# Kernel optimization log

Measured on AMD Instinct MI355X. Metric: run time of the kernel, lower is better.

Reference implementation:

```python
import jax, jax.numpy as jnp
import numpy as np

N, E, D, H = 20000, 160000, 64, 4  # nodes, edges, hidden_dim, heads
C = D  # per-head out channels (concat=False -> mean over heads)
NEG_SLOPE = 0.2


def _mlp2(x, w1, b1, w2, b2):
    return jax.nn.relu(x @ w1 + b1) @ w2 + b2


def _gatv2(h, e_full, src, dst, wl, bl, wr, br, we, att, bias):
    # GATv2Conv (PyG semantics, share_weights=False, concat=False)
    xl = (h @ wl + bl).reshape(N, H, C)          # lin_l (source / message features)
    xr = (h @ wr + br).reshape(N, H, C)          # lin_r (target features)
    ee = (e_full @ we).reshape(-1, H, C)         # lin_edge (no bias)
    m = jax.nn.leaky_relu(xl[src] + xr[dst] + ee, NEG_SLOPE)  # [E',H,C]
    logits = jnp.einsum('ehc,hc->eh', m, att)    # [E',H]
    # segment softmax over destination node neighborhoods
    mx = jax.ops.segment_max(logits, dst, num_segments=N)
    ex = jnp.exp(logits - mx[dst])
    s = jax.ops.segment_sum(ex, dst, num_segments=N)
    alpha = ex / s[dst]                          # [E',H]
    out = jax.ops.segment_sum(xl[src] * alpha[..., None], dst, num_segments=N)
    return out.mean(axis=1) + bias               # [N,D]


def setup_inputs() -> dict:
    key = jax.random.key(0)
    ks = iter(jax.random.split(key, 40))
    nrm = lambda shape, s=0.05: jax.random.normal(next(ks), shape, jnp.float32) * s
    inp = {
        'x': jax.random.normal(next(ks), (N, 2), jnp.float32),
        'edge_index': jax.random.randint(next(ks), (2, E), 0, N, dtype=jnp.int32),
        'edge_attr': jax.random.normal(next(ks), (E, 3), jnp.float32),
        # node encoder
        'ne_w1': nrm((2, D)), 'ne_b1': jnp.zeros((D,), jnp.float32),
        'ne_w2': nrm((D, D)), 'ne_b2': jnp.zeros((D,), jnp.float32),
        # edge encoder
        'ee_w1': nrm((3, D)), 'ee_b1': jnp.zeros((D,), jnp.float32),
        'ee_w2': nrm((D, D)), 'ee_b2': jnp.zeros((D,), jnp.float32),
        # 3 GATv2Conv layers, params stacked along leading layer dim
        'cv_wl': nrm((3, D, H * C)), 'cv_bl': jnp.zeros((3, H * C), jnp.float32),
        'cv_wr': nrm((3, D, H * C)), 'cv_br': jnp.zeros((3, H * C), jnp.float32),
        'cv_we': nrm((3, D, H * C)),
        'cv_att': nrm((3, H, C)),
        'cv_bias': jnp.zeros((3, D), jnp.float32),
        # edge classifier (3D -> D -> 1)
        'ec_w1': nrm((3 * D, D)), 'ec_b1': jnp.zeros((D,), jnp.float32),
        'ec_w2': nrm((D, 1)), 'ec_b2': jnp.zeros((1,), jnp.float32),
        'or_w1': nrm((D, D)), 'or_b1': jnp.zeros((D,), jnp.float32),
        'or_w2': nrm((D, 2)), 'or_b2': jnp.zeros((2,), jnp.float32),
    }
    return inp


def reference(x, edge_index, edge_attr,
              ne_w1, ne_b1, ne_w2, ne_b2,
              ee_w1, ee_b1, ee_w2, ee_b2,
              cv_wl, cv_bl, cv_wr, cv_br, cv_we, cv_att, cv_bias,
              ec_w1, ec_b1, ec_w2, ec_b2,
              or_w1, or_b1, or_w2, or_b2):
    src, dst = edge_index[0], edge_index[1]
    h = _mlp2(x, ne_w1, ne_b1, ne_w2, ne_b2)          # [N,D]
    e = _mlp2(edge_attr, ee_w1, ee_b1, ee_w2, ee_b2)  # [E,D]
    # PyG add_self_loops with fill_value='mean': loop attr = mean of incoming edge attrs
    cnt = jax.ops.segment_sum(jnp.ones((E,), e.dtype), dst, num_segments=N)
    e_loop = jax.ops.segment_sum(e, dst, num_segments=N) / jnp.clip(cnt, 1.0)[:, None]
    loop = jnp.arange(N, dtype=src.dtype)
    src_f = jnp.concatenate([src, loop])
    dst_f = jnp.concatenate([dst, loop])
    e_f = jnp.concatenate([e, e_loop], axis=0)        # [E+N,D]
    for l in range(3):
        h = h + jax.nn.relu(_gatv2(h, e_f, src_f, dst_f,
                                   cv_wl[l], cv_bl[l], cv_wr[l], cv_br[l],
                                   cv_we[l], cv_att[l], cv_bias[l]))
    edge_feat = jnp.concatenate([h[src], h[dst], e], axis=1)  # [E,3D]
    edge_scores = jax.nn.sigmoid(_mlp2(edge_feat, ec_w1, ec_b1, ec_w2, ec_b2)).squeeze(-1)
    pred_offsets = _mlp2(h, or_w1, or_b1, or_w2, or_b2)       # [N,2]
    return (edge_scores, pred_offsets)
```

## Files before the change

### kernel.cpp

```cpp
#include <hip/hip_runtime.h>

#define N_NODES 20000
#define N_EDGES 160000
#define EP (N_EDGES + N_NODES)
#define NBLK ((N_NODES + 255) / 256)
#define PREP_SEG 16384
#define EENC_BLK (N_EDGES / 64)
#define ECLS_BLK (N_EDGES / 64)

typedef __attribute__((ext_vector_type(8))) short bf16x8;
typedef __attribute__((ext_vector_type(4))) float f32x4;

__device__ __forceinline__ short f2bf(float f) {
  unsigned u = __float_as_uint(f);
  unsigned r = (u + 0x7FFFu + ((u >> 16) & 1u)) >> 16;
  return (short)r;
}
__device__ __forceinline__ float b2f(short s) {
  return __uint_as_float(((unsigned)(unsigned short)s) << 16);
}

__device__ __forceinline__ f32x4 mfma16(bf16x8 a, bf16x8 b, f32x4 c) {
  return __builtin_amdgcn_mfma_f32_16x16x32_bf16(a, b, c, 0, 0, 0);
}

__device__ __forceinline__ float bcast(float v, int k) {
  return __uint_as_float(__builtin_amdgcn_readlane(__float_as_uint(v), k));
}

__device__ __forceinline__ float wred_sum(float v) {
#pragma unroll
  for (int o = 32; o > 0; o >>= 1) v += __shfl_xor(v, o, 64);
  return v;
}

__device__ __forceinline__ void gl16(const short* g, short* l) {
  __builtin_amdgcn_global_load_lds(
      (const __attribute__((address_space(1))) void*)g,
      (__attribute__((address_space(3))) void*)l, 16, 0, 0);
}

__global__ void k_prep_all(const float* __restrict__ cv_wl, const float* __restrict__ cv_wr,
                           const float* __restrict__ cv_we, const float* __restrict__ ec_w1,
                           const float* __restrict__ ee_w2,
                           short* __restrict__ wlf, short* __restrict__ wrf,
                           short* __restrict__ wef, short* __restrict__ updf,
                           short* __restrict__ eclsf, short* __restrict__ encf,
                           int* __restrict__ cnt, int* __restrict__ fill) {
  int i = blockIdx.x * 256 + threadIdx.x;
  if (i < 12 * PREP_SEG) {
    int grp = i / PREP_SEG;
    int r = i % PREP_SEG;
    int kind = grp / 3, l = grp % 3;
    int j = r & 7, lane = (r >> 3) & 63;
    int q = lane & 15, g = lane >> 4;
    if (kind < 3) {
      int kh = (r >> 9) & 1, t = (r >> 10) & 3, w = r >> 12;
      int k = kh * 32 + g * 8 + j, c = w * 64 + t * 16 + q;
      const float* W = (kind == 0 ? cv_wl : kind == 1 ? cv_wr : cv_we) + (size_t)l * 64 * 256;
      short* out = (kind == 0 ? wlf : kind == 1 ? wrf : wef) + (size_t)l * PREP_SEG;
      out[r] = f2bf(W[k * 256 + c]);
    } else {
      int kh = (r >> 9) & 7, w = r >> 12;
      int k = kh * 32 + g * 8 + j, c = w * 16 + q;
      const float* W = cv_wl + (size_t)l * 64 * 256;
      updf[(size_t)l * PREP_SEG + r] = f2bf(0.25f * W[(k & 63) * 256 + (k >> 6) * 64 + c]);
    }
  } else if (i < 12 * PREP_SEG + 12288) {
    int r = i - 12 * PREP_SEG;
    int j = r & 7, lane = (r >> 3) & 63, f = r >> 9;
    int w = f / 6, kh = f % 6;
    int q = lane & 15, g = lane >> 4;
    int k = kh * 32 + g * 8 + j, c = w * 16 + q;
    eclsf[r] = f2bf(ec_w1[(size_t)k * 64 + c]);
  } else if (i < 12 * PREP_SEG + 12288 + 4096) {
    int r = i - 12 * PREP_SEG - 12288;
    int j = r & 7, lane = (r >> 3) & 63, f = r >> 9;
    int w = f >> 1, kh = f & 1;
    int q = lane & 15, g = lane >> 4;
    int k = kh * 32 + g * 8 + j, c = w * 16 + q;
    encf[r] = f2bf(ee_w2[(size_t)k * 64 + c]);
  } else {
    int r = i - (12 * PREP_SEG + 12288 + 4096);
    if (r < N_NODES) cnt[r] = 0;
    else if (r < 2 * N_NODES) fill[r - N_NODES] = 0;
  }
}


__global__ void k_count(const int* __restrict__ dst, int* __restrict__ cnt) {
  int i = blockIdx.x * blockDim.x + threadIdx.x;
  if (i < N_EDGES) atomicAdd(&cnt[dst[i]], 1);
}

__global__ void k_scan1(const int* __restrict__ cnt, int* __restrict__ row_ptr,
                        int* __restrict__ bsum) {
  __shared__ int sh[256];
  int t = threadIdx.x, b = blockIdx.x, i = b * 256 + t;
  int v = (i < N_NODES) ? cnt[i] + 1 : 0;
  sh[t] = v;
  __syncthreads();
#pragma unroll
  for (int off = 1; off < 256; off <<= 1) {
    int x = (t >= off) ? sh[t - off] : 0;
    __syncthreads();
    sh[t] += x;
    __syncthreads();
  }
  if (i < N_NODES) row_ptr[i + 1] = sh[t];
  if (t == 255) bsum[b] = sh[255];
}

__global__ void k_scan2(const int* __restrict__ bsum, int* __restrict__ boff) {
  __shared__ int sh[256];
  int t = threadIdx.x;
  int v = (t < NBLK) ? bsum[t] : 0;
  sh[t] = v;
  __syncthreads();
#pragma unroll
  for (int off = 1; off < 256; off <<= 1) {
    int x = (t >= off) ? sh[t - off] : 0;
    __syncthreads();
    sh[t] += x;
    __syncthreads();
  }
  if (t < NBLK) boff[t] = sh[t] - v;
}

__global__ void k_scan3(const int* __restrict__ boff, int* __restrict__ row_ptr) {
  int t = threadIdx.x, b = blockIdx.x, i = b * 256 + t;
  if (i < N_NODES) row_ptr[i + 1] += boff[b];
  if (i == 0) row_ptr[0] = 0;
}

__global__ void k_scatter(const int* __restrict__ dst, const int* __restrict__ row_ptr,
                          int* __restrict__ fill, int* __restrict__ col_idx,
                          int* __restrict__ pdst) {
  int i = blockIdx.x * blockDim.x + threadIdx.x;
  if (i >= EP) return;
  int d = (i < N_EDGES) ? dst[i] : (i - N_EDGES);
  int p = row_ptr[d] + atomicAdd(&fill[d], 1);
  col_idx[p] = i;
  pdst[p] = d;
}

__global__ void k_sortp(const int* __restrict__ row_ptr, int* __restrict__ col_idx,
                        const int* __restrict__ src, int* __restrict__ psrc,
                        int* __restrict__ pos) {
  int n = blockIdx.x * blockDim.x + threadIdx.x;
  if (n >= N_NODES) return;
  int s = row_ptr[n], e = row_ptr[n + 1];
  for (int i = s + 1; i < e; ++i) {
    int v = col_idx[i];
    int j = i - 1;
    while (j >= s && col_idx[j] > v) { col_idx[j + 1] = col_idx[j]; --j; }
    col_idx[j + 1] = v;
  }
  for (int i = s; i < e; ++i) {
    int eid = col_idx[i];
    pos[eid] = i;
    psrc[i] = (eid < N_EDGES) ? src[eid] : (eid - N_EDGES);
  }
}


__global__ __launch_bounds__(256) void k_enc(
    const float* __restrict__ x,
    const float* __restrict__ nw1, const float* __restrict__ nb1,
    const float* __restrict__ nw2, const float* __restrict__ nb2,
    const float* __restrict__ ea,
    const float* __restrict__ ew1, const float* __restrict__ eb1,
    const short* __restrict__ encf, const float* __restrict__ eb2,
    const int* __restrict__ pos, short* __restrict__ efc,
    float* __restrict__ h, short* __restrict__ hb) {
  __shared__ __align__(16) char smraw[17920];
  int tid = threadIdx.x;
  int lane = tid & 63, w = tid >> 6, q = lane & 15, g = lane >> 4;
  if (blockIdx.x < EENC_BLK) {
    short* hs = (short*)smraw;
    short* ot = (short*)(smraw + 9216);
    int* ps = (int*)(smraw + 9216 + 8192);
    int e0 = blockIdx.x * 64;
    if (tid < 64) ps[tid] = pos[e0 + tid];
    float w1a = ew1[lane], w1b = ew1[64 + lane], w1c = ew1[128 + lane], b1v = eb1[lane];
#pragma unroll
    for (int t = 0; t < 16; ++t) {
      int e = w * 16 + t;
      float a0 = ea[(size_t)(e0 + e) * 3];
      float a1 = ea[(size_t)(e0 + e) * 3 + 1];
      float a2 = ea[(size_t)(e0 + e) * 3 + 2];
      float hid = fmaxf(a0 * w1a + a1 * w1b + a2 * w1c + b1v, 0.f);
      hs[e * 72 + lane] = f2bf(hid);
    }
    bf16x8 A0 = *(const bf16x8*)&hs[(w * 16 + q) * 72 + g * 8];
    bf16x8 A1 = *(const bf16x8*)&hs[(w * 16 + q) * 72 + 32 + g * 8];
#pragma unroll
    for (int cc = 0; cc < 4; ++cc) {
      bf16x8 B0 = *(const bf16x8*)(encf + ((size_t)(cc * 2 + 0) * 64 + lane) * 8);
      bf16x8 B1 = *(const bf16x8*)(encf + ((size_t)(cc * 2 + 1) * 64 + lane) * 8);
      f32x4 z = {0.f, 0.f, 0.f, 0.f};
      z = mfma16(A0, B0, z);
      z = mfma16(A1, B1, z);
      float bv = eb2[cc * 16 + q];
#pragma unroll
      for (int r = 0; r < 4; ++r)
        ot[(w * 16 + g * 4 + r) * 64 + cc * 16 + q] = f2bf(z[r] + bv);
    }
    __syncthreads();
    int row = tid >> 2, part = tid & 3;
    short* d = efc + (size_t)ps[row] * 64 + part * 16;
    const short* s = ot + row * 64 + part * 16;
    *(bf16x8*)d = *(const bf16x8*)s;
    *(bf16x8*)(d + 8) = *(const bf16x8*)(s + 8);
  } else {
    float* w2l = (float*)smraw;
#pragma unroll
    for (int qq = 0; qq < 16; ++qq) w2l[qq * 256 + tid] = nw2[qq * 256 + tid];
    __syncthreads();
    int n = (blockIdx.x - EENC_BLK) * 4 + w;
    float x0 = x[n * 2], x1 = x[n * 2 + 1];
    float hid = fmaxf(x0 * nw1[lane] + x1 * nw1[64 + lane] + nb1[lane], 0.f);
    float out = nb2[lane];
#pragma unroll
    for (int k = 0; k < 64; ++k) out += bcast(hid, k) * w2l[k * 64 + lane];
    h[n * 64 + lane] = out;
    hb[n * 64 + lane] = f2bf(out);
  }
}

__global__ __launch_bounds__(256) void k_loop_feat(
    const int* __restrict__ row_ptr, short* __restrict__ efc) {
  int tid = threadIdx.x, lane = tid & 63, w = tid >> 6;
  int n = blockIdx.x * 4 + w;
  int s = row_ptr[n], e1 = row_ptr[n + 1];
  int r8 = lane >> 3, oct = lane & 7;
  float acc[8];
#pragma unroll
  for (int j = 0; j < 8; ++j) acc[j] = 0.f;
  for (int p0 = s; p0 < e1 - 1; p0 += 8) {
    int p = p0 + r8;
    if (p < e1 - 1) {
      bf16x8 A = *(const bf16x8*)(efc + (size_t)p * 64 + oct * 8);
#pragma unroll
      for (int j = 0; j < 8; ++j) acc[j] += b2f(A[j]);
    }
  }
#pragma unroll
  for (int j = 0; j < 8; ++j) {
    acc[j] += __shfl_xor(acc[j], 8, 64);
    acc[j] += __shfl_xor(acc[j], 16, 64);
    acc[j] += __shfl_xor(acc[j], 32, 64);
  }
  int c = e1 - 1 - s;
  float invc = 1.f / (float)(c > 0 ? c : 1);
  if (lane < 8) {
    bf16x8 o8;
#pragma unroll
    for (int j = 0; j < 8; ++j) o8[j] = f2bf(acc[j] * invc);
    *(bf16x8*)(efc + (size_t)(e1 - 1) * 64 + lane * 8) = o8;
  }
}


__global__ __launch_bounds__(256) void k_elog(
    const short* __restrict__ hb, const short* __restrict__ efc,
    const int* __restrict__ psrc, const int* __restrict__ pdst,
    const short* __restrict__ wlf, const short* __restrict__ wrf,
    const short* __restrict__ wef, const float* __restrict__ bl,
    const float* __restrict__ br, const float* __restrict__ att, float* __restrict__ lg) {
  __shared__ __align__(16) short smA[96 * 2 * 64];
  int tid = threadIdx.x;
  int w = tid >> 6, lane = tid & 63, q = lane & 15, g = lane >> 4;
  int cbase = w * 64;
  int pb = blockIdx.x * 96;

  int id6[6];
#pragma unroll
  for (int j = 0; j < 6; ++j) {
    int s = (w * 6 + j) * 64 + lane;
    int t = s >> 8, s2 = s & 255;
    int r = s2 >> 7, e = (s2 >> 3) & 15;
    int pe = pb + t * 16 + e;
    id6[j] = (r == 0) ? psrc[pe] : pe;
  }
#pragma unroll
  for (int j = 0; j < 6; ++j) {
    int s = (w * 6 + j) * 64 + lane;
    int s2 = s & 255;
    int r = s2 >> 7, e = (s2 >> 3) & 15, c16 = s & 7;
    int cs = (c16 ^ (e & 7)) * 8;
    const short* gp = ((r == 1) ? efc : hb) + (size_t)id6[j] * 64 + cs;
    gl16(gp, &smA[(size_t)s * 8]);
  }

  int nd[6];
#pragma unroll
  for (int t = 0; t < 6; ++t) nd[t] = pdst[pb + t * 16 + q];

  bf16x8 Bl[4][2], Br[4][2], Be[4][2];
  float av[4], bv[4];
#pragma unroll
  for (int t = 0; t < 4; ++t) {
    int c = cbase + t * 16 + q;
    av[t] = att[c];
    bv[t] = bl[c] + br[c];
#pragma unroll
    for (int kh = 0; kh < 2; ++kh) {
      size_t fo = ((size_t)((w * 4 + t) * 2 + kh) * 64 + lane) * 8;
      Bl[t][kh] = *(const bf16x8*)(wlf + fo);
      Br[t][kh] = *(const bf16x8*)(wrf + fo);
      Be[t][kh] = *(const bf16x8*)(wef + fo);
    }
  }
  __syncthreads();

  int xa = (g ^ (q & 7)) * 8;
  int xb = ((4 + g) ^ (q & 7)) * 8;
  int rowoff = q * 64;
#pragma unroll
  for (int t = 0; t < 6; ++t) {
    const short* base = smA + t * 2048;
    const short* ar = hb + (size_t)nd[t] * 64;
    bf16x8 As0 = *(const bf16x8*)(base + rowoff + xa);
    bf16x8 As1 = *(const bf16x8*)(base + rowoff + xb);
    bf16x8 Ar0 = *(const bf16x8*)(ar + g * 8);
    bf16x8 Ar1 = *(const bf16x8*)(ar + 32 + g * 8);
    bf16x8 Ae0 = *(const bf16x8*)(base + 1024 + rowoff + xa);
    bf16x8 Ae1 = *(const bf16x8*)(base + 1024 + rowoff + xb);
    f32x4 acc[4];
#pragma unroll
    for (int tt = 0; tt < 4; ++tt) {
      f32x4 z = {0.f, 0.f, 0.f, 0.f};
      z = mfma16(As0, Bl[tt][0], z);
      z = mfma16(As1, Bl[tt][1], z);
      z = mfma16(Ar0, Br[tt][0], z);
      z = mfma16(Ar1, Br[tt][1], z);
      z = mfma16(Ae0, Be[tt][0], z);
      acc[tt] = mfma16(Ae1, Be[tt][1], z);
    }
#pragma unroll
    for (int r = 0; r < 4; ++r) {
      float pd = 0.f;
#pragma unroll
      for (int tt = 0; tt < 4; ++tt) {
        float m = acc[tt][r] + bv[tt];
        m = m > 0.f ? m : 0.2f * m;
        pd += m * av[tt];
      }
      pd += __shfl_xor(pd, 1, 64);
      pd += __shfl_xor(pd, 2, 64);
      pd += __shfl_xor(pd, 4, 64);
      pd += __shfl_xor(pd, 8, 64);
      if (q == 0) lg[(size_t)(pb + t * 16 + g * 4 + r) * 4 + w] = pd;
    }
  }
}

__global__ __launch_bounds__(256) void k_aggupd(
    const short* __restrict__ hbin, const float* __restrict__ lg,
    const int* __restrict__ row_ptr, const int* __restrict__ psrc,
    const short* __restrict__ updf, const float* __restrict__ bl,
    const float* __restrict__ bias, float* __restrict__ h, short* __restrict__ hbout) {
  __shared__ short agls[16 * 264];
  __shared__ float albuf[4][260];
  int tid = threadIdx.x, lane = tid & 63, w = tid >> 6;
  int q = lane & 15, g = lane >> 4;
  int n0 = blockIdx.x * 16;
  int i16 = lane & 15, h4 = lane >> 4;
  float* alw = albuf[w];
#pragma unroll 1
  for (int i = 0; i < 4; ++i) {
    int n = n0 + w * 4 + i;
    int s0 = row_ptr[n], s1 = row_ptr[n + 1];
    float m = -3.4e38f;
    for (int p = s0 + i16; p < s1; p += 16) m = fmaxf(m, lg[(size_t)p * 4 + h4]);
#pragma unroll
    for (int o = 1; o < 16; o <<= 1) m = fmaxf(m, __shfl_xor(m, o, 64));
    float sum = 0.f;
    for (int p = s0 + i16; p < s1; p += 16) sum += __expf(lg[(size_t)p * 4 + h4] - m);
#pragma unroll
    for (int o = 1; o < 16; o <<= 1) sum += __shfl_xor(sum, o, 64);
    float inv = 1.f / sum;
    float ih4[4];
#pragma unroll
    for (int hh = 0; hh < 4; ++hh) ih4[hh] = __shfl(inv, hh * 16, 64);
    float acc[4][4];
#pragma unroll
    for (int hh = 0; hh < 4; ++hh)
#pragma unroll
      for (int j = 0; j < 4; ++j) acc[hh][j] = 0.f;
    for (int wst = s0; wst < s1; wst += 64) {
      int wend = wst + 64 < s1 ? wst + 64 : s1;
#pragma unroll
      for (int k = 0; k < 4; ++k) {
        int p = wst + k * 16 + i16;
        float e = (p < s1) ? __expf(lg[(size_t)p * 4 + h4] - m) : 0.f;
        alw[(k * 16 + i16) * 4 + h4] = e;
      }
      asm volatile("s_waitcnt lgkmcnt(0)" ::: "memory");
      for (int p0 = wst; p0 < wend; p0 += 4) {
        int p = p0 + h4;
        bool v = p < wend;
        int pc = v ? p : wend - 1;
        int sp = psrc[pc];
        float4 al = *(const float4*)&alw[(pc - wst) * 4];
        short4 hv = *(const short4*)(hbin + (size_t)sp * 64 + i16 * 4);
        if (!v) { al.x = 0.f; al.y = 0.f; al.z = 0.f; al.w = 0.f; }
        float hf0 = b2f(hv.x), hf1 = b2f(hv.y), hf2 = b2f(hv.z), hf3 = b2f(hv.w);
        acc[0][0] += al.x * hf0; acc[0][1] += al.x * hf1;
        acc[0][2] += al.x * hf2; acc[0][3] += al.x * hf3;
        acc[1][0] += al.y * hf0; acc[1][1] += al.y * hf1;
        acc[1][2] += al.y * hf2; acc[1][3] += al.y * hf3;
        acc[2][0] += al.z * hf0; acc[2][1] += al.z * hf1;
        acc[2][2] += al.z * hf2; acc[2][3] += al.z * hf3;
        acc[3][0] += al.w * hf0; acc[3][1] += al.w * hf1;
        acc[3][2] += al.w * hf2; acc[3][3] += al.w * hf3;
      }
    }
#pragma unroll
    for (int hh = 0; hh < 4; ++hh)
#pragma unroll
      for (int j = 0; j < 4; ++j) {
        acc[hh][j] += __shfl_xor(acc[hh][j], 16, 64);
        acc[hh][j] += __shfl_xor(acc[hh][j], 32, 64);
      }
    if (lane < 16) {
#pragma unroll
      for (int hh = 0; hh < 4; ++hh) {
        short4 o4;
        o4.x = f2bf(acc[hh][0] * ih4[hh]);
        o4.y = f2bf(acc[hh][1] * ih4[hh]);
        o4.z = f2bf(acc[hh][2] * ih4[hh]);
        o4.w = f2bf(acc[hh][3] * ih4[hh]);
        *(short4*)(agls + (w * 4 + i) * 264 + hh * 64 + i16 * 4) = o4;
      }
    }
  }
  __syncthreads();
  const short* arow = agls + q * 264;
  f32x4 z = {0.f, 0.f, 0.f, 0.f};
#pragma unroll
  for (int kh = 0; kh < 8; ++kh) {
    bf16x8 A = *(const bf16x8*)(arow + kh * 32 + g * 8);
    bf16x8 B = *(const bf16x8*)(updf + ((size_t)(w * 8 + kh) * 64 + lane) * 8);
    z = mfma16(A, B, z);
  }
  int c = w * 16 + q;
  float bf = 0.25f * (bl[c] + bl[64 + c] + bl[128 + c] + bl[192 + c]) + bias[c];
#pragma unroll
  for (int r = 0; r < 4; ++r) {
    int n = n0 + g * 4 + r;
    float nh = h[(size_t)n * 64 + c] + fmaxf(z[r] + bf, 0.f);
    h[(size_t)n * 64 + c] = nh;
    hbout[(size_t)n * 64 + c] = f2bf(nh);
  }
}

__global__ __launch_bounds__(256) void k_heads(
    const short* __restrict__ hb, const short* __restrict__ efc,
    const int* __restrict__ src, const int* __restrict__ dst,
    const int* __restrict__ pos, const short* __restrict__ eclsf,
    const float* __restrict__ b1, const float* __restrict__ w2,
    const float* __restrict__ b2,
    const float* __restrict__ h, const float* __restrict__ ow1,
    const float* __restrict__ ob1, const float* __restrict__ ow2,
    const float* __restrict__ ob2, float* __restrict__ out) {
  __shared__ __align__(16) char smraw[25600];
  int tid = threadIdx.x;
  int w = tid >> 6, lane = tid & 63, q = lane & 15, g = lane >> 4;
  if (blockIdx.x < ECLS_BLK) {
    short* smA = (short*)smraw;
    float* sm = (float*)(smraw + 24576);
    int e0b = blockIdx.x * 64;
    int id6[6];
#pragma unroll
    for (int j = 0; j < 6; ++j) {
      int s = (w * 6 + j) * 64 + lane;
      int r = s >> 9, e = (s >> 3) & 63;
      int eg = e0b + e;
      id6[j] = (r == 0) ? src[eg] : (r == 1) ? dst[eg] : pos[eg];
    }
#pragma unroll
    for (int j = 0; j < 6; ++j) {
      int s = (w * 6 + j) * 64 + lane;
      int r = s >> 9, e = (s >> 3) & 63, c16 = s & 7;
      int cs = (c16 ^ (e & 7)) * 8;
      const short* gp = ((r == 2) ? efc : hb) + (size_t)id6[j] * 64 + cs;
      gl16(gp, &smA[(size_t)s * 8]);
    }
    int c = w * 16 + q;
    bf16x8 Bf[6];
#pragma unroll
    for (int kh = 0; kh < 6; ++kh)
      Bf[kh] = *(const bf16x8*)(eclsf + ((size_t)(w * 6 + kh) * 64 + lane) * 8);
    float b1v = b1[c], w2v = w2[c], b2v = b2[0];
    __syncthreads();
    int xa = (g ^ (q & 7)) * 8;
    int xb = ((4 + g) ^ (q & 7)) * 8;
#pragma unroll
    for (int tile = 0; tile < 4; ++tile) {
      const short* rp = smA + (tile * 16 + q) * 64;
      f32x4 acc = {0.f, 0.f, 0.f, 0.f};
      acc = mfma16(*(const bf16x8*)(rp + xa), Bf[0], acc);
      acc = mfma16(*(const bf16x8*)(rp + xb), Bf[1], acc);
      acc = mfma16(*(const bf16x8*)(rp + 4096 + xa), Bf[2], acc);
      acc = mfma16(*(const bf16x8*)(rp + 4096 + xb), Bf[3], acc);
      acc = mfma16(*(const bf16x8*)(rp + 8192 + xa), Bf[4], acc);
      acc = mfma16(*(const bf16x8*)(rp + 8192 + xb), Bf[5], acc);
#pragma unroll
      for (int r = 0; r < 4; ++r) {
        float hv = fmaxf(acc[r] + b1v, 0.f) * w2v;
        hv += __shfl_xor(hv, 1, 64);
        hv += __shfl_xor(hv, 2, 64);
        hv += __shfl_xor(hv, 4, 64);
        hv += __shfl_xor(hv, 8, 64);
        if (q == 0) sm[tile * 64 + w * 16 + g * 4 + r] = hv;
      }
    }
    __syncthreads();
    if (tid < 64) {
      int tile = tid >> 4, e = tid & 15;
      float t = sm[tile * 64 + e] + sm[tile * 64 + 16 + e] +
                sm[tile * 64 + 32 + e] + sm[tile * 64 + 48 + e] + b2v;
      out[e0b + tile * 16 + e] = 1.f / (1.f + __expf(-t));
    }
  } else {
    float* w1l = (float*)smraw;
#pragma unroll
    for (int qq = 0; qq < 16; ++qq) w1l[qq * 256 + tid] = ow1[qq * 256 + tid];
    __syncthreads();
    int n = (blockIdx.x - ECLS_BLK) * 4 + w;
    float hr = h[n * 64 + lane];
    float hid = ob1[lane];
#pragma unroll
    for (int k = 0; k < 64; ++k) hid += bcast(hr, k) * w1l[k * 64 + lane];
    hid = fmaxf(hid, 0.f);
    float p0 = wred_sum(hid * ow2[lane * 2]);
    float p1 = wred_sum(hid * ow2[lane * 2 + 1]);
    if (lane == 0) {
      out[N_EDGES + n * 2] = p0 + ob2[0];
      out[N_EDGES + n * 2 + 1] = p1 + ob2[1];
    }
  }
}


extern "C" void kernel_launch(void* const* d_in, const int* in_sizes, int n_in,
                              void* d_out, int out_size, void* d_ws, size_t ws_size,
                              hipStream_t stream) {
  const float* x     = (const float*)d_in[0];
  const int*   eidx  = (const int*)d_in[1];
  const float* eattr = (const float*)d_in[2];
  const float* ne_w1 = (const float*)d_in[3];
  const float* ne_b1 = (const float*)d_in[4];
  const float* ne_w2 = (const float*)d_in[5];
  const float* ne_b2 = (const float*)d_in[6];
  const float* ee_w1 = (const float*)d_in[7];
  const float* ee_b1 = (const float*)d_in[8];
  const float* ee_w2 = (const float*)d_in[9];
  const float* ee_b2 = (const float*)d_in[10];
  const float* cv_wl = (const float*)d_in[11];
  const float* cv_bl = (const float*)d_in[12];
  const float* cv_wr = (const float*)d_in[13];
  const float* cv_br = (const float*)d_in[14];
  const float* cv_we = (const float*)d_in[15];
  const float* cv_att = (const float*)d_in[16];
  const float* cv_bias = (const float*)d_in[17];
  const float* ec_w1 = (const float*)d_in[18];
  const float* ec_b1 = (const float*)d_in[19];
  const float* ec_w2 = (const float*)d_in[20];
  const float* ec_b2 = (const float*)d_in[21];
  const float* or_w1 = (const float*)d_in[22];
  const float* or_b1 = (const float*)d_in[23];
  const float* or_w2 = (const float*)d_in[24];
  const float* or_b2 = (const float*)d_in[25];

  const int* src = eidx;
  const int* dst = eidx + N_EDGES;

  float* fws = (float*)d_ws;
  size_t o = 0;
  float* h  = fws + o; o += (size_t)N_NODES * 64;
  float* lg = fws + o; o += (size_t)EP * 4;
  short* sws = (short*)(fws + o);
  size_t so = 0;
  short* hb0  = sws + so; so += (size_t)N_NODES * 64;
  short* hb1  = sws + so; so += (size_t)N_NODES * 64;
  short* efc  = sws + so; so += (size_t)EP * 64;
  short* wlf  = sws + so; so += 3 * PREP_SEG;
  short* wrf  = sws + so; so += 3 * PREP_SEG;
  short* wef  = sws + so; so += 3 * PREP_SEG;
  short* updf = sws + so; so += 3 * PREP_SEG;
  short* eclsf = sws + so; so += 12288;
  short* encf  = sws + so; so += 4096;
  int* iws = (int*)(sws + so + (so & 1));
  int* row_ptr = iws;
  int* col_idx = iws + (N_NODES + 64);
  int* pdst = col_idx + EP;
  int* psrc = pdst + EP;
  int* pos  = psrc + EP;
  int* cnt  = pos + EP;
  int* fill = cnt + N_NODES;
  int* bsum = fill + N_NODES;
  int* boff = bsum + 128;

  float* out = (float*)d_out;

  k_prep_all<<<(12 * PREP_SEG + 12288 + 4096 + 2 * N_NODES + 255) / 256, 256, 0, stream>>>(
      cv_wl, cv_wr, cv_we, ec_w1, ee_w2, wlf, wrf, wef, updf, eclsf, encf, cnt, fill);

  k_count<<<(N_EDGES + 255) / 256, 256, 0, stream>>>(dst, cnt);
  k_scan1<<<NBLK, 256, 0, stream>>>(cnt, row_ptr, bsum);
  k_scan2<<<1, 256, 0, stream>>>(bsum, boff);
  k_scan3<<<NBLK, 256, 0, stream>>>(boff, row_ptr);
  k_scatter<<<(EP + 255) / 256, 256, 0, stream>>>(dst, row_ptr, fill, col_idx, pdst);
  k_sortp<<<(N_NODES + 255) / 256, 256, 0, stream>>>(row_ptr, col_idx, src, psrc, pos);

  k_enc<<<EENC_BLK + N_NODES / 4, 256, 0, stream>>>(
      x, ne_w1, ne_b1, ne_w2, ne_b2, eattr, ee_w1, ee_b1, encf, ee_b2, pos, efc, h, hb0);
  k_loop_feat<<<N_NODES / 4, 256, 0, stream>>>(row_ptr, efc);

  short* hcur = hb0;
  short* hnxt = hb1;
  for (int l = 0; l < 3; ++l) {
    const float* bl = cv_bl + (size_t)l * 256;
    const float* br = cv_br + (size_t)l * 256;
    const float* at = cv_att + (size_t)l * 256;
    const float* bi = cv_bias + (size_t)l * 64;
    k_elog<<<EP / 96, 256, 0, stream>>>(hcur, efc, psrc, pdst,
                                        wlf + (size_t)l * PREP_SEG,
                                        wrf + (size_t)l * PREP_SEG,
                                        wef + (size_t)l * PREP_SEG, bl, br, at, lg);
    k_aggupd<<<N_NODES / 16, 256, 0, stream>>>(hcur, lg, row_ptr, psrc,
                                               updf + (size_t)l * PREP_SEG, bl, bi, h, hnxt);
    short* tmp = hcur; hcur = hnxt; hnxt = tmp;
  }

  k_heads<<<ECLS_BLK + N_NODES / 4, 256, 0, stream>>>(
      hcur, efc, src, dst, pos, eclsf, ec_b1, ec_w2, ec_b2,
      h, or_w1, or_b1, or_w2, or_b2, out);
}
```

Baseline: 283.9 us.

## Fuse scan kernels, stage edge attrs in LDS, fold softmax sum into aggregation

Merges the second and third prefix-scan kernels into one single-block kernel that applies block offsets to row_ptr, removing one launch. The edge encoder loads edge attributes cooperatively into shared memory instead of doing strided per-thread global loads. The aggregation kernel computes the softmax denominator during the weighted-sum pass rather than in a separate pass over the logits. Leaky ReLU becomes fmaxf. The single-block offset pass runs serially over 20000 entries on one CU, which may cost more than the launch it removes.

New measurement: 283.8 us, median of 2. Within noise of the previous version (-0.0%).

```diff
diff --git a/kernel.cpp b/kernel.cpp
--- a/kernel.cpp
+++ b/kernel.cpp
@@ -111,8 +111,9 @@
   if (t == 255) bsum[b] = sh[255];
 }
 
-__global__ void k_scan2(const int* __restrict__ bsum, int* __restrict__ boff) {
+__global__ void k_scan23(const int* __restrict__ bsum, int* __restrict__ row_ptr) {
   __shared__ int sh[256];
+  __shared__ int boffs[128];
   int t = threadIdx.x;
   int v = (t < NBLK) ? bsum[t] : 0;
   sh[t] = v;
@@ -124,13 +125,10 @@
     sh[t] += x;
     __syncthreads();
   }
-  if (t < NBLK) boff[t] = sh[t] - v;
-}
-
-__global__ void k_scan3(const int* __restrict__ boff, int* __restrict__ row_ptr) {
-  int t = threadIdx.x, b = blockIdx.x, i = b * 256 + t;
-  if (i < N_NODES) row_ptr[i + 1] += boff[b];
-  if (i == 0) row_ptr[0] = 0;
+  if (t < NBLK) boffs[t] = sh[t] - v;
+  __syncthreads();
+  for (int i = t; i < N_NODES; i += 256) row_ptr[i + 1] += boffs[i >> 8];
+  if (t == 0) row_ptr[0] = 0;
 }
 
 __global__ void k_scatter(const int* __restrict__ dst, const int* __restrict__ row_ptr,
@@ -173,22 +171,23 @@
     const short* __restrict__ encf, const float* __restrict__ eb2,
     const int* __restrict__ pos, short* __restrict__ efc,
     float* __restrict__ h, short* __restrict__ hb) {
-  __shared__ __align__(16) char smraw[17920];
+  __shared__ __align__(16) char smraw[18432];
   int tid = threadIdx.x;
   int lane = tid & 63, w = tid >> 6, q = lane & 15, g = lane >> 4;
   if (blockIdx.x < EENC_BLK) {
     short* hs = (short*)smraw;
     short* ot = (short*)(smraw + 9216);
-    int* ps = (int*)(smraw + 9216 + 8192);
+    int* ps = (int*)(smraw + 17408);
+    float* easm = (float*)(smraw + 17664);
     int e0 = blockIdx.x * 64;
     if (tid < 64) ps[tid] = pos[e0 + tid];
+    if (tid < 192) easm[tid] = ea[(size_t)e0 * 3 + tid];
     float w1a = ew1[lane], w1b = ew1[64 + lane], w1c = ew1[128 + lane], b1v = eb1[lane];
+    __syncthreads();
 #pragma unroll
     for (int t = 0; t < 16; ++t) {
       int e = w * 16 + t;
-      float a0 = ea[(size_t)(e0 + e) * 3];
-      float a1 = ea[(size_t)(e0 + e) * 3 + 1];
-      float a2 = ea[(size_t)(e0 + e) * 3 + 2];
+      float a0 = easm[e * 3], a1 = easm[e * 3 + 1], a2 = easm[e * 3 + 2];
       float hid = fmaxf(a0 * w1a + a1 * w1b + a2 * w1c + b1v, 0.f);
       hs[e * 72 + lane] = f2bf(hid);
     }
@@ -344,7 +343,7 @@
 #pragma unroll
       for (int tt = 0; tt < 4; ++tt) {
         float m = acc[tt][r] + bv[tt];
-        m = m > 0.f ? m : 0.2f * m;
+        m = fmaxf(m, 0.2f * m);
         pd += m * av[tt];
       }
       pd += __shfl_xor(pd, 1, 64);
@@ -377,13 +376,6 @@
 #pragma unroll
     for (int o = 1; o < 16; o <<= 1) m = fmaxf(m, __shfl_xor(m, o, 64));
     float sum = 0.f;
-    for (int p = s0 + i16; p < s1; p += 16) sum += __expf(lg[(size_t)p * 4 + h4] - m);
-#pragma unroll
-    for (int o = 1; o < 16; o <<= 1) sum += __shfl_xor(sum, o, 64);
-    float inv = 1.f / sum;
-    float ih4[4];
-#pragma unroll
-    for (int hh = 0; hh < 4; ++hh) ih4[hh] = __shfl(inv, hh * 16, 64);
     float acc[4][4];
 #pragma unroll
     for (int hh = 0; hh < 4; ++hh)
@@ -396,6 +388,7 @@
         int p = wst + k * 16 + i16;
         float e = (p < s1) ? __expf(lg[(size_t)p * 4 + h4] - m) : 0.f;
         alw[(k * 16 + i16) * 4 + h4] = e;
+        sum += e;
       }
       asm volatile("s_waitcnt lgkmcnt(0)" ::: "memory");
       for (int p0 = wst; p0 < wend; p0 += 4) {
@@ -417,6 +410,12 @@
         acc[3][2] += al.w * hf2; acc[3][3] += al.w * hf3;
       }
     }
+#pragma unroll
+    for (int o = 1; o < 16; o <<= 1) sum += __shfl_xor(sum, o, 64);
+    float inv = 1.f / sum;
+    float ih4[4];
+#pragma unroll
+    for (int hh = 0; hh < 4; ++hh) ih4[hh] = __shfl(inv, hh * 16, 64);
 #pragma unroll
     for (int hh = 0; hh < 4; ++hh)
 #pragma unroll
@@ -602,7 +601,6 @@
   int* cnt  = pos + EP;
   int* fill = cnt + N_NODES;
   int* bsum = fill + N_NODES;
-  int* boff = bsum + 128;
 
   float* out = (float*)d_out;
 
@@ -611,8 +609,7 @@
 
   k_count<<<(N_EDGES + 255) / 256, 256, 0, stream>>>(dst, cnt);
   k_scan1<<<NBLK, 256, 0, stream>>>(cnt, row_ptr, bsum);
-  k_scan2<<<1, 256, 0, stream>>>(bsum, boff);
-  k_scan3<<<NBLK, 256, 0, stream>>>(boff, row_ptr);
+  k_scan23<<<1, 256, 0, stream>>>(bsum, row_ptr);
   k_scatter<<<(EP + 255) / 256, 256, 0, stream>>>(dst, row_ptr, fill, col_idx, pdst);
   k_sortp<<<(N_NODES + 255) / 256, 256, 0, stream>>>(row_ptr, col_idx, src, psrc, pos);
 
```
